# Kernel tuning notes

Hardware: AMD Instinct MI355X
Metric: run time of the kernel (lower is better)

The kernel has to match this reference:

```python
import jax, jax.numpy as jnp
import numpy as np

T, B, C = 1024, 8, 1024
H, K, P = 16, 7, 3  # num_heads, kernel_size, padding_l
R = C // H


def setup_inputs() -> dict:
    key = jax.random.key(0)
    k1, k2, k3, k4 = jax.random.split(key, 4)
    x = jax.random.normal(k1, (T, B, C), dtype=jnp.float32)
    # weight_linear: Linear(C -> H*K) with bias
    lim = 1.0 / np.sqrt(C)
    W_lin = jax.random.uniform(k2, (H * K, C), minval=-lim, maxval=lim, dtype=jnp.float32)
    b_lin = jax.random.uniform(k3, (H * K,), minval=-lim, maxval=lim, dtype=jnp.float32)
    conv_bias = jnp.zeros((C,), dtype=jnp.float32)
    return {"x": x, "W_lin": W_lin, "b_lin": b_lin, "conv_bias": conv_bias}


def reference(x, W_lin, b_lin, conv_bias):
    # per-position dynamic filters: (T, B, H*K)
    w = jnp.einsum('tbc,oc->tbo', x, W_lin) + b_lin
    # weight_softmax=True, renorm_padding=False: softmax over kernel dim
    w = jax.nn.softmax(w.reshape(T * B * H, K), axis=-1)
    # (T, B*H, K) -> (B*H, T, K)
    w = w.reshape(T, B * H, K).transpose(1, 0, 2)
    # x as (B*H, T, R)
    xv = x.reshape(T, B * H, R).transpose(1, 0, 2)
    # band-matrix bmm == sliding window: out[t] = sum_k w[t,k] * x[t - P + k]
    x_pad = jnp.pad(xv, ((0, 0), (P, K - 1 - P), (0, 0)))
    windows = jnp.stack([x_pad[:, k:k + T] for k in range(K)], axis=2)  # (BH, T, K, R)
    out = jnp.einsum('btk,btkr->btr', w, windows)  # (BH, T, R)
    out = out.transpose(1, 0, 2).reshape(T, B, C)
    return out + conv_bias[None, None, :]
```

## Files before the change

kernel.cpp:

```cpp
#include <hip/hip_runtime.h>
#include <stdint.h>

#define T_DIM 1024
#define B_DIM 8
#define C_DIM 1024
#define H_DIM 16
#define K_SZ  7
#define P_PAD 3
#define O_DIM (H_DIM * K_SZ)
#define TB    (T_DIM * B_DIM)

typedef __attribute__((ext_vector_type(8))) short bf16x8;
typedef __attribute__((ext_vector_type(4))) float f32x4;
typedef __attribute__((ext_vector_type(4))) uint32_t u32x4;

union FragU { uint32_t u[4]; bf16x8 v; };

__device__ inline uint32_t pk_bf16(float a, float b) {
  uint32_t ua = __float_as_uint(a), ub = __float_as_uint(b);
  ua += 0x7FFFu + ((ua >> 16) & 1u);
  ub += 0x7FFFu + ((ub >> 16) & 1u);
  return (ua >> 16) | (ub & 0xFFFF0000u);
}

__device__ inline bf16x8 load_bf16x8_cvt(const float* __restrict__ p) {
  float4 lo = *reinterpret_cast<const float4*>(p);
  float4 hi = *reinterpret_cast<const float4*>(p + 4);
  FragU f;
  f.u[0] = pk_bf16(lo.x, lo.y);
  f.u[1] = pk_bf16(lo.z, lo.w);
  f.u[2] = pk_bf16(hi.x, hi.y);
  f.u[3] = pk_bf16(hi.z, hi.w);
  return f.v;
}

__device__ inline void bar_lds() {
  __builtin_amdgcn_sched_barrier(0);
  asm volatile("s_waitcnt lgkmcnt(0)" ::: "memory");
  __builtin_amdgcn_s_barrier();
  __builtin_amdgcn_sched_barrier(0);
}

__global__ __launch_bounds__(256) void prep_wfrag_kernel(
    const float* __restrict__ Wl, uint16_t* __restrict__ Wf) {
  const int t  = blockIdx.x * 256 + threadIdx.x;
  const int f  = t >> 6;
  const int l  = t & 63;
  const int ks = f / 7;
  const int nf = f - ks * 7;
  const int row = nf * 16 + (l & 15);
  const int kb  = ks * 32 + (l >> 4) * 8;
  bf16x8 v = load_bf16x8_cvt(Wl + (size_t)row * C_DIM + kb);
  *reinterpret_cast<bf16x8*>(Wf + (size_t)t * 8) = v;
}

template <bool PREPPED>
__global__ __launch_bounds__(1024, 4) void fused_pipe_kernel(
    const float* __restrict__ x, const float* __restrict__ Wl,
    const uint16_t* __restrict__ Wf, const float* __restrict__ bl,
    const float* __restrict__ cb, float* __restrict__ out) {
  __shared__ char  ring[32 * 2048];
  __shared__ float part[2][16][116];
  __shared__ float wsm[16][17][8];

  const int tid  = threadIdx.x;
  const int wv   = tid >> 6;
  const int lane = tid & 63;
  const int l15  = lane & 15;
  const int oct  = lane >> 4;

  const int bid = blockIdx.x;
  const int xcd = bid & 7;
  const int r8  = bid >> 3;
  const int b   = r8 >> 2;
  const int t0  = (xcd * 4 + (r8 & 3)) * 32;

  auto stage_write = [&](int task, int gbase) {
    const int q   = task >> 7;
    const int c16 = task & 127;
    const int g   = min(max(gbase + q, 0), T_DIM - 1);
    const float* __restrict__ src =
        x + ((size_t)(g * B_DIM + b)) * C_DIM + c16 * 8;
    float4 v0 = *reinterpret_cast<const float4*>(src);
    float4 v1 = *reinterpret_cast<const float4*>(src + 4);
    FragU f;
    f.u[0] = pk_bf16(v0.x, v0.y);
    f.u[1] = pk_bf16(v0.z, v0.w);
    f.u[2] = pk_bf16(v1.x, v1.y);
    f.u[3] = pk_bf16(v1.z, v1.w);
    const int dst = (g & 31) * 2048 + ((c16 * 16) ^ ((g & 7) << 4));
    *reinterpret_cast<bf16x8*>(ring + dst) = f.v;
  };

  auto mfma_phase = [&](int wbase) {
    if (wv < 14) {
      const int kh = (wv >= 7) ? 1 : 0;
      const int nf = wv - kh * 7;
      f32x4 acc = (f32x4)(0.f);
      const int ag   = wbase + l15;
      const char* ab = ring + (ag & 31) * 2048;
      const int axor = (ag & 7) << 4;
#pragma unroll
      for (int s = 0; s < 16; ++s) {
        const int ksg = kh * 16 + s;
        bf16x8 a = *reinterpret_cast<const bf16x8*>(
            ab + ((ksg * 64 + oct * 16) ^ axor));
        bf16x8 bf;
        if (PREPPED)
          bf = *reinterpret_cast<const bf16x8*>(
              Wf + ((size_t)((ksg * 7 + nf) * 64) + lane) * 8);
        else
          bf = load_bf16x8_cvt(Wl + (size_t)(nf * 16 + l15) * C_DIM + ksg * 32 + oct * 8);
        acc = __builtin_amdgcn_mfma_f32_16x16x32_bf16(a, bf, acc, 0, 0, 0);
      }
#pragma unroll
      for (int rr = 0; rr < 4; ++rr)
        part[kh][oct * 4 + rr][nf * 16 + l15] = acc[rr];
    }
  };

  auto softmax_phase = [&]() {
    if (tid < 256) {
      const int row = tid >> 4;
      const int h   = tid & 15;
      float lg[7];
      float m = -1e30f;
#pragma unroll
      for (int j = 0; j < 7; ++j) {
        const int c = h * 7 + j;
        float s_ = part[0][row][c] + part[1][row][c] + bl[c];
        lg[j] = s_;
        m = fmaxf(m, s_);
      }
      float s = 0.f;
#pragma unroll
      for (int j = 0; j < 7; ++j) { lg[j] = __expf(lg[j] - m); s += lg[j]; }
      const float inv = 1.0f / s;
#pragma unroll
      for (int j = 0; j < 7; ++j) wsm[row][h][j] = lg[j] * inv;
    }
  };

  auto conv_phase = [&](int wbase) {
    const int row  = wv;
    const int gout = wbase + row;
    float okf[7];
    int slotb[7], sxor[7];
#pragma unroll
    for (int j = 0; j < 7; ++j) {
      const int tp = gout + j - P_PAD;
      okf[j] = (tp >= 0 && tp < T_DIM) ? 1.f : 0.f;
      const int g = min(max(tp, 0), T_DIM - 1);
      slotb[j] = (g & 31) * 2048;
      sxor[j]  = (g & 7) << 4;
    }
    float* __restrict__ obase = out + ((size_t)(gout * B_DIM + b)) * C_DIM;
#pragma unroll
    for (int ii = 0; ii < 2; ++ii) {
      const int ch0  = ii * 512 + lane * 8;
      const int head = ch0 >> 6;
      float4 w0 = *reinterpret_cast<const float4*>(&wsm[row][head][0]);
      float4 w1 = *reinterpret_cast<const float4*>(&wsm[row][head][4]);
      const float wj[7] = {w0.x, w0.y, w0.z, w0.w, w1.x, w1.y, w1.z};
      float4 c0 = *reinterpret_cast<const float4*>(cb + ch0);
      float4 c1 = *reinterpret_cast<const float4*>(cb + ch0 + 4);
      float a0 = c0.x, a1 = c0.y, a2 = c0.z, a3 = c0.w;
      float a4 = c1.x, a5 = c1.y, a6 = c1.z, a7 = c1.w;
#pragma unroll
      for (int j = 0; j < 7; ++j) {
        const float w = wj[j] * okf[j];
        const u32x4 d = *reinterpret_cast<const u32x4*>(
            ring + slotb[j] + ((ch0 * 2) ^ sxor[j]));
        a0 += w * __uint_as_float(d.x << 16);
        a1 += w * __uint_as_float(d.x & 0xffff0000u);
        a2 += w * __uint_as_float(d.y << 16);
        a3 += w * __uint_as_float(d.y & 0xffff0000u);
        a4 += w * __uint_as_float(d.z << 16);
        a5 += w * __uint_as_float(d.z & 0xffff0000u);
        a6 += w * __uint_as_float(d.w << 16);
        a7 += w * __uint_as_float(d.w & 0xffff0000u);
      }
      *reinterpret_cast<float4*>(obase + ch0)     = make_float4(a0, a1, a2, a3);
      *reinterpret_cast<float4*>(obase + ch0 + 4) = make_float4(a4, a5, a6, a7);
    }
  };

#pragma unroll
  for (int it = 0; it < 3; ++it) {
    const int task = tid + it * 1024;
    if (task < 22 * 128) stage_write(task, t0 - 3);
  }
  bar_lds();

  float4 pf0, pf1, pf2, pf3;
  {
    const int q0 = tid >> 7, c0_ = tid & 127;
    const int g0 = min(t0 + 19 + q0, T_DIM - 1);
    const float* __restrict__ s0 =
        x + ((size_t)(g0 * B_DIM + b)) * C_DIM + c0_ * 8;
    pf0 = *reinterpret_cast<const float4*>(s0);
    pf1 = *reinterpret_cast<const float4*>(s0 + 4);
    const int t2 = tid + 1024;
    const int q1 = t2 >> 7, c1_ = t2 & 127;
    const int g1 = min(t0 + 19 + q1, T_DIM - 1);
    const float* __restrict__ s1 =
        x + ((size_t)(g1 * B_DIM + b)) * C_DIM + c1_ * 8;
    pf2 = *reinterpret_cast<const float4*>(s1);
    pf3 = *reinterpret_cast<const float4*>(s1 + 4);
  }

  mfma_phase(t0);
  bar_lds();
  softmax_phase();
  bar_lds();
  conv_phase(t0);
  bar_lds();

  {
    const int q0 = tid >> 7, c0_ = tid & 127;
    const int g0 = min(t0 + 19 + q0, T_DIM - 1);
    FragU f;
    f.u[0] = pk_bf16(pf0.x, pf0.y);
    f.u[1] = pk_bf16(pf0.z, pf0.w);
    f.u[2] = pk_bf16(pf1.x, pf1.y);
    f.u[3] = pk_bf16(pf1.z, pf1.w);
    *reinterpret_cast<bf16x8*>(
        ring + (g0 & 31) * 2048 + ((c0_ * 16) ^ ((g0 & 7) << 4))) = f.v;
    const int t2 = tid + 1024;
    const int q1 = t2 >> 7, c1_ = t2 & 127;
    const int g1 = min(t0 + 19 + q1, T_DIM - 1);
    FragU f2;
    f2.u[0] = pk_bf16(pf2.x, pf2.y);
    f2.u[1] = pk_bf16(pf2.z, pf2.w);
    f2.u[2] = pk_bf16(pf3.x, pf3.y);
    f2.u[3] = pk_bf16(pf3.z, pf3.w);
    *reinterpret_cast<bf16x8*>(
        ring + (g1 & 31) * 2048 + ((c1_ * 16) ^ ((g1 & 7) << 4))) = f2.v;
  }
  bar_lds();

  mfma_phase(t0 + 16);
  bar_lds();
  softmax_phase();
  bar_lds();
  conv_phase(t0 + 16);
}

extern "C" void kernel_launch(void* const* d_in, const int* in_sizes, int n_in,
                              void* d_out, int out_size, void* d_ws, size_t ws_size,
                              hipStream_t stream) {
  const float* x  = (const float*)d_in[0];
  const float* Wl = (const float*)d_in[1];
  const float* bl = (const float*)d_in[2];
  const float* cb = (const float*)d_in[3];
  float* out = (float*)d_out;

  const bool prepped = ws_size >= 262144;

  if (prepped) {
    uint16_t* wf = (uint16_t*)d_ws;
    prep_wfrag_kernel<<<(32 * 7 * 64) / 256, 256, 0, stream>>>(Wl, wf);
    fused_pipe_kernel<true><<<256, 1024, 0, stream>>>(x, Wl, wf, bl, cb, out);
  } else {
    fused_pipe_kernel<false><<<256, 1024, 0, stream>>>(x, Wl, nullptr, bl, cb, out);
  }
}
```

Before: 29.67 us.

## Stage x rows into LDS as fp32 via direct global-to-LDS DMA

Replaces the register-based load, bf16 pack and LDS write staging of x with global_load_lds DMA that keeps fp32 rows in a swizzled LDS ring (the ring doubles to 128KB). The MFMA phase now converts to bf16 when it reads A fragments, and the conv phase uses fp32 data directly with nontemporal stores. The second-half prefetch becomes per-wave DMA with vmcnt waits in place of register prefetch. The goal is to cut VGPR traffic and conversion work on the load path. The cost is a larger LDS footprint, which lowers occupancy, plus conversion repeated per MFMA read.

After: 30.13 us. Within noise of the previous version (+1.6%).

```diff
diff --git a/kernel.cpp b/kernel.cpp
--- a/kernel.cpp
+++ b/kernel.cpp
@@ -12,7 +12,6 @@
 
 typedef __attribute__((ext_vector_type(8))) short bf16x8;
 typedef __attribute__((ext_vector_type(4))) float f32x4;
-typedef __attribute__((ext_vector_type(4))) uint32_t u32x4;
 
 union FragU { uint32_t u[4]; bf16x8 v; };
 
@@ -23,21 +22,46 @@
   return (ua >> 16) | (ub & 0xFFFF0000u);
 }
 
+__device__ inline bf16x8 cvt8(f32x4 lo, f32x4 hi) {
+  FragU f;
+  f.u[0] = pk_bf16(lo[0], lo[1]);
+  f.u[1] = pk_bf16(lo[2], lo[3]);
+  f.u[2] = pk_bf16(hi[0], hi[1]);
+  f.u[3] = pk_bf16(hi[2], hi[3]);
+  return f.v;
+}
+
 __device__ inline bf16x8 load_bf16x8_cvt(const float* __restrict__ p) {
-  float4 lo = *reinterpret_cast<const float4*>(p);
-  float4 hi = *reinterpret_cast<const float4*>(p + 4);
-  FragU f;
-  f.u[0] = pk_bf16(lo.x, lo.y);
-  f.u[1] = pk_bf16(lo.z, lo.w);
-  f.u[2] = pk_bf16(hi.x, hi.y);
-  f.u[3] = pk_bf16(hi.z, hi.w);
-  return f.v;
-}
-
+  f32x4 lo = *reinterpret_cast<const f32x4*>(p);
+  f32x4 hi = *reinterpret_cast<const f32x4*>(p + 4);
+  return cvt8(lo, hi);
+}
+
+__device__ inline void gload_lds16(const void* g, void* l) {
+  __builtin_amdgcn_global_load_lds(
+      (const __attribute__((address_space(1))) uint32_t*)g,
+      (__attribute__((address_space(3))) uint32_t*)l, 16, 0, 0);
+}
+
+__device__ inline void sbar() {
+  __builtin_amdgcn_sched_barrier(0);
+  __builtin_amdgcn_s_barrier();
+  __builtin_amdgcn_sched_barrier(0);
+}
 __device__ inline void bar_lds() {
   __builtin_amdgcn_sched_barrier(0);
   asm volatile("s_waitcnt lgkmcnt(0)" ::: "memory");
   __builtin_amdgcn_s_barrier();
+  __builtin_amdgcn_sched_barrier(0);
+}
+__device__ inline void vm0() {
+  __builtin_amdgcn_sched_barrier(0);
+  asm volatile("s_waitcnt vmcnt(0)" ::: "memory");
+  __builtin_amdgcn_sched_barrier(0);
+}
+__device__ inline void vm4() {
+  __builtin_amdgcn_sched_barrier(0);
+  asm volatile("s_waitcnt vmcnt(4)" ::: "memory");
   __builtin_amdgcn_sched_barrier(0);
 }
 
@@ -55,11 +79,11 @@
 }
 
 template <bool PREPPED>
-__global__ __launch_bounds__(1024, 4) void fused_pipe_kernel(
+__global__ __launch_bounds__(1024) void fused_dma_kernel(
     const float* __restrict__ x, const float* __restrict__ Wl,
     const uint16_t* __restrict__ Wf, const float* __restrict__ bl,
     const float* __restrict__ cb, float* __restrict__ out) {
-  __shared__ char  ring[32 * 2048];
+  __shared__ float ring[32 * 1024];
   __shared__ float part[2][16][116];
   __shared__ float wsm[16][17][8];
 
@@ -75,47 +99,47 @@
   const int b   = r8 >> 2;
   const int t0  = (xcd * 4 + (r8 & 3)) * 32;
 
-  auto stage_write = [&](int task, int gbase) {
-    const int q   = task >> 7;
-    const int c16 = task & 127;
-    const int g   = min(max(gbase + q, 0), T_DIM - 1);
-    const float* __restrict__ src =
-        x + ((size_t)(g * B_DIM + b)) * C_DIM + c16 * 8;
-    float4 v0 = *reinterpret_cast<const float4*>(src);
-    float4 v1 = *reinterpret_cast<const float4*>(src + 4);
-    FragU f;
-    f.u[0] = pk_bf16(v0.x, v0.y);
-    f.u[1] = pk_bf16(v0.z, v0.w);
-    f.u[2] = pk_bf16(v1.x, v1.y);
-    f.u[3] = pk_bf16(v1.z, v1.w);
-    const int dst = (g & 31) * 2048 + ((c16 * 16) ^ ((g & 7) << 4));
-    *reinterpret_cast<bf16x8*>(ring + dst) = f.v;
+  auto stage_dma = [&](int ridx) {
+    const int tlog = t0 - 3 + ridx;
+    const int g    = min(max(tlog, 0), T_DIM - 1);
+    const int slot = tlog & 31;
+    const int key  = (tlog & 7) << 4;
+    const char* __restrict__ rowp =
+        (const char*)(x + ((size_t)(g * B_DIM + b)) * C_DIM);
+    char* ldsrow = (char*)ring + slot * 4096;
+#pragma unroll
+    for (int q = 0; q < 4; ++q) {
+      gload_lds16(rowp + (((q * 1024) + lane * 16) ^ key), ldsrow + q * 1024);
+    }
   };
 
   auto mfma_phase = [&](int wbase) {
     if (wv < 14) {
       const int kh = (wv >= 7) ? 1 : 0;
       const int nf = wv - kh * 7;
-      f32x4 acc = (f32x4)(0.f);
-      const int ag   = wbase + l15;
-      const char* ab = ring + (ag & 31) * 2048;
-      const int axor = (ag & 7) << 4;
+      const int tA = wbase + l15;
+      const char* rowb = (const char*)ring + (tA & 31) * 4096;
+      const int key = (tA & 7) << 4;
+      f32x4 acc0 = (f32x4)(0.f), acc1 = (f32x4)(0.f);
 #pragma unroll
       for (int s = 0; s < 16; ++s) {
-        const int ksg = kh * 16 + s;
-        bf16x8 a = *reinterpret_cast<const bf16x8*>(
-            ab + ((ksg * 64 + oct * 16) ^ axor));
+        const int ksg   = kh * 16 + s;
+        const int inrow = ksg * 128 + oct * 32;
+        f32x4 lo = *reinterpret_cast<const f32x4*>(rowb + (inrow ^ key));
+        f32x4 hi = *reinterpret_cast<const f32x4*>(rowb + ((inrow + 16) ^ key));
+        bf16x8 a = cvt8(lo, hi);
         bf16x8 bf;
         if (PREPPED)
           bf = *reinterpret_cast<const bf16x8*>(
               Wf + ((size_t)((ksg * 7 + nf) * 64) + lane) * 8);
         else
           bf = load_bf16x8_cvt(Wl + (size_t)(nf * 16 + l15) * C_DIM + ksg * 32 + oct * 8);
-        acc = __builtin_amdgcn_mfma_f32_16x16x32_bf16(a, bf, acc, 0, 0, 0);
+        if (s < 8) acc0 = __builtin_amdgcn_mfma_f32_16x16x32_bf16(a, bf, acc0, 0, 0, 0);
+        else       acc1 = __builtin_amdgcn_mfma_f32_16x16x32_bf16(a, bf, acc1, 0, 0, 0);
       }
 #pragma unroll
       for (int rr = 0; rr < 4; ++rr)
-        part[kh][oct * 4 + rr][nf * 16 + l15] = acc[rr];
+        part[kh][oct * 4 + rr][nf * 16 + l15] = acc0[rr] + acc1[rr];
     }
   };
 
@@ -144,70 +168,42 @@
   auto conv_phase = [&](int wbase) {
     const int row  = wv;
     const int gout = wbase + row;
+    const char* tbase[7];
+    int tkey[7];
     float okf[7];
-    int slotb[7], sxor[7];
 #pragma unroll
     for (int j = 0; j < 7; ++j) {
       const int tp = gout + j - P_PAD;
       okf[j] = (tp >= 0 && tp < T_DIM) ? 1.f : 0.f;
       const int g = min(max(tp, 0), T_DIM - 1);
-      slotb[j] = (g & 31) * 2048;
-      sxor[j]  = (g & 7) << 4;
+      tbase[j] = (const char*)ring + (g & 31) * 4096;
+      tkey[j]  = (g & 7) << 4;
     }
     float* __restrict__ obase = out + ((size_t)(gout * B_DIM + b)) * C_DIM;
 #pragma unroll
-    for (int ii = 0; ii < 2; ++ii) {
-      const int ch0  = ii * 512 + lane * 8;
-      const int head = ch0 >> 6;
+    for (int k = 0; k < 4; ++k) {
+      const int inrow = k * 1024 + lane * 16;
+      const int ch    = k * 256 + lane * 4;
+      const int head  = k * 4 + oct;
       float4 w0 = *reinterpret_cast<const float4*>(&wsm[row][head][0]);
       float4 w1 = *reinterpret_cast<const float4*>(&wsm[row][head][4]);
-      const float wj[7] = {w0.x, w0.y, w0.z, w0.w, w1.x, w1.y, w1.z};
-      float4 c0 = *reinterpret_cast<const float4*>(cb + ch0);
-      float4 c1 = *reinterpret_cast<const float4*>(cb + ch0 + 4);
-      float a0 = c0.x, a1 = c0.y, a2 = c0.z, a3 = c0.w;
-      float a4 = c1.x, a5 = c1.y, a6 = c1.z, a7 = c1.w;
+      const float wj[7] = {w0.x * okf[0], w0.y * okf[1], w0.z * okf[2],
+                           w0.w * okf[3], w1.x * okf[4], w1.y * okf[5],
+                           w1.z * okf[6]};
+      f32x4 a = *reinterpret_cast<const f32x4*>(cb + ch);
 #pragma unroll
       for (int j = 0; j < 7; ++j) {
-        const float w = wj[j] * okf[j];
-        const u32x4 d = *reinterpret_cast<const u32x4*>(
-            ring + slotb[j] + ((ch0 * 2) ^ sxor[j]));
-        a0 += w * __uint_as_float(d.x << 16);
-        a1 += w * __uint_as_float(d.x & 0xffff0000u);
-        a2 += w * __uint_as_float(d.y << 16);
-        a3 += w * __uint_as_float(d.y & 0xffff0000u);
-        a4 += w * __uint_as_float(d.z << 16);
-        a5 += w * __uint_as_float(d.z & 0xffff0000u);
-        a6 += w * __uint_as_float(d.w << 16);
-        a7 += w * __uint_as_float(d.w & 0xffff0000u);
+        f32x4 d = *reinterpret_cast<const f32x4*>(tbase[j] + (inrow ^ tkey[j]));
+        a += wj[j] * d;
       }
-      *reinterpret_cast<float4*>(obase + ch0)     = make_float4(a0, a1, a2, a3);
-      *reinterpret_cast<float4*>(obase + ch0 + 4) = make_float4(a4, a5, a6, a7);
-    }
-  };
-
-#pragma unroll
-  for (int it = 0; it < 3; ++it) {
-    const int task = tid + it * 1024;
-    if (task < 22 * 128) stage_write(task, t0 - 3);
-  }
-  bar_lds();
-
-  float4 pf0, pf1, pf2, pf3;
-  {
-    const int q0 = tid >> 7, c0_ = tid & 127;
-    const int g0 = min(t0 + 19 + q0, T_DIM - 1);
-    const float* __restrict__ s0 =
-        x + ((size_t)(g0 * B_DIM + b)) * C_DIM + c0_ * 8;
-    pf0 = *reinterpret_cast<const float4*>(s0);
-    pf1 = *reinterpret_cast<const float4*>(s0 + 4);
-    const int t2 = tid + 1024;
-    const int q1 = t2 >> 7, c1_ = t2 & 127;
-    const int g1 = min(t0 + 19 + q1, T_DIM - 1);
-    const float* __restrict__ s1 =
-        x + ((size_t)(g1 * B_DIM + b)) * C_DIM + c1_ * 8;
-    pf2 = *reinterpret_cast<const float4*>(s1);
-    pf3 = *reinterpret_cast<const float4*>(s1 + 4);
-  }
+      __builtin_nontemporal_store(a, reinterpret_cast<f32x4*>(obase + ch));
+    }
+  };
+
+  for (int r = wv; r < 22; r += 16) stage_dma(r);
+  if (wv >= 6) stage_dma(16 + wv);
+  if (wv < 6) vm0(); else vm4();
+  sbar();
 
   mfma_phase(t0);
   bar_lds();
@@ -216,28 +212,8 @@
   conv_phase(t0);
   bar_lds();
 
-  {
-    const int q0 = tid >> 7, c0_ = tid & 127;
-    const int g0 = min(t0 + 19 + q0, T_DIM - 1);
-    FragU f;
-    f.u[0] = pk_bf16(pf0.x, pf0.y);
-    f.u[1] = pk_bf16(pf0.z, pf0.w);
-    f.u[2] = pk_bf16(pf1.x, pf1.y);
-    f.u[3] = pk_bf16(pf1.z, pf1.w);
-    *reinterpret_cast<bf16x8*>(
-        ring + (g0 & 31) * 2048 + ((c0_ * 16) ^ ((g0 & 7) << 4))) = f.v;
-    const int t2 = tid + 1024;
-    const int q1 = t2 >> 7, c1_ = t2 & 127;
-    const int g1 = min(t0 + 19 + q1, T_DIM - 1);
-    FragU f2;
-    f2.u[0] = pk_bf16(pf2.x, pf2.y);
-    f2.u[1] = pk_bf16(pf2.z, pf2.w);
-    f2.u[2] = pk_bf16(pf3.x, pf3.y);
-    f2.u[3] = pk_bf16(pf3.z, pf3.w);
-    *reinterpret_cast<bf16x8*>(
-        ring + (g1 & 31) * 2048 + ((c1_ * 16) ^ ((g1 & 7) << 4))) = f2.v;
-  }
-  bar_lds();
+  if (wv < 6) { stage_dma(32 + wv); vm0(); }
+  sbar();
 
   mfma_phase(t0 + 16);
   bar_lds();
@@ -260,8 +236,8 @@
   if (prepped) {
     uint16_t* wf = (uint16_t*)d_ws;
     prep_wfrag_kernel<<<(32 * 7 * 64) / 256, 256, 0, stream>>>(Wl, wf);
-    fused_pipe_kernel<true><<<256, 1024, 0, stream>>>(x, Wl, wf, bl, cb, out);
+    fused_dma_kernel<true><<<256, 1024, 0, stream>>>(x, Wl, wf, bl, cb, out);
   } else {
-    fused_pipe_kernel<false><<<256, 1024, 0, stream>>>(x, Wl, nullptr, bl, cb, out);
+    fused_dma_kernel<false><<<256, 1024, 0, stream>>>(x, Wl, nullptr, bl, cb, out);
   }
 }
```
